# Kernel tuning notes

Measured on AMD Instinct MI355X. Metric: run time of the kernel, lower is better.

Reference implementation:

```python
import jax, jax.numpy as jnp
import numpy as np

B, N, C = 4, 262144, 10
K_PRE, K_POST = 4096, 500          # before_nms_max, after_nms_max
ROI_THR, NMS_THR = 0.1, 0.01       # roi_threshold, nms_threshold


def setup_inputs() -> dict:
    key = jax.random.key(0)
    k1, k2, k3, k4 = jax.random.split(key, 4)
    # raw logits; sigmoid(-2 + noise) straddles roi_threshold=0.1 realistically
    cls = jax.random.normal(k1, (B, N, C), jnp.float32) - 2.0
    centers = jax.random.uniform(k2, (B, N, 3), jnp.float32, minval=-50.0, maxval=50.0)
    sizes = jax.random.uniform(k3, (B, N, 3), jnp.float32, minval=0.5, maxval=5.0)
    heading = jax.random.uniform(k4, (B, N, 1), jnp.float32, minval=-np.pi, maxval=np.pi)
    boxes = jnp.concatenate([centers, sizes, heading], axis=-1)  # (B, N, 7)
    return {"batch_cls_preds": cls, "batch_box_preds": boxes}


def _pairwise_bev_iou(b):
    # b: (K, 7) = [x, y, z, dx, dy, dz, heading]; BEV IoU (heading ignored,
    # axis-aligned approximation of the rotated-IoU CUDA kernel).
    x, y, dx, dy = b[:, 0], b[:, 1], b[:, 3], b[:, 4]
    x1, x2 = x - dx * 0.5, x + dx * 0.5
    y1, y2 = y - dy * 0.5, y + dy * 0.5
    ix = jnp.clip(jnp.minimum(x2[:, None], x2[None, :]) - jnp.maximum(x1[:, None], x1[None, :]), 0.0)
    iy = jnp.clip(jnp.minimum(y2[:, None], y2[None, :]) - jnp.maximum(y1[:, None], y1[None, :]), 0.0)
    inter = ix * iy                              # (K, K)
    area = dx * dy                               # (K,)
    union = area[:, None] + area[None, :] - inter
    return inter / jnp.maximum(union, 1e-6)


def _nms_one(scores, labels, boxes):
    # scores: (N,), labels: (N,) int32, boxes: (N, 7)
    s = jnp.where(scores > ROI_THR, scores, -1.0)       # score-threshold filter
    topv, topi = jax.lax.top_k(s, K_PRE)                # keep top before_nms_max
    tb = boxes[topi]                                     # (K_PRE, 7)
    tl = labels[topi]
    iou = _pairwise_bev_iou(tb)                          # (K_PRE, K_PRE)
    keep0 = topv > ROI_THR

    def body(i, keep):
        # a kept higher-score box i suppresses later boxes with IoU > thr
        sup = (iou[i] > NMS_THR) & (jnp.arange(K_PRE) > i) & keep[i]
        return keep & ~sup

    keep = jax.lax.fori_loop(0, K_PRE, body, keep0)
    kept_scores = jnp.where(keep, topv, -1.0)
    fv, fi = jax.lax.top_k(kept_scores, K_POST)          # after_nms_max slots
    m = fv > 0.0
    final_scores = jnp.where(m, fv, 0.0)                 # (K_POST,)
    final_boxes = tb[fi] * m[:, None].astype(tb.dtype)   # (K_POST, 7)
    final_labels = jnp.where(m, tl[fi], -1)              # (K_POST,)
    return final_scores, final_boxes, final_labels


def reference(batch_cls_preds, batch_box_preds):
    probs = jax.nn.sigmoid(batch_cls_preds)              # (B, N, C)
    scores = jnp.max(probs, axis=-1)                     # per-anchor best class score
    labels = jnp.argmax(probs, axis=-1).astype(jnp.int32)
    final_scores, final_boxes, final_labels = jax.vmap(_nms_one)(scores, labels, batch_box_preds)
    return final_scores, final_boxes, final_labels
```

## Files before the change

kernel.cpp:

```cpp
#include <hip/hip_runtime.h>
#include <stdint.h>

constexpr int B = 4;
constexpr int N = 262144;
constexpr int C = 10;
constexpr int KPRE = 4096;
constexpr int KPOST = 500;
constexpr float ROI_THR = 0.1f;
constexpr float NMS_THR = 0.01f;
constexpr int CAP = 8192;
constexpr int MASKW = KPRE / 64;
constexpr int RJT = 2;
constexpr int MAXP = 32;

__device__ __forceinline__ uint32_t f2k(float f) {
  uint32_t u = __float_as_uint(f);
  return (u & 0x80000000u) ? ~u : (u | 0x80000000u);
}
__device__ __forceinline__ float k2f(uint32_t k) {
  uint32_t u = (k & 0x80000000u) ? (k ^ 0x80000000u) : ~k;
  return __uint_as_float(u);
}
__device__ __forceinline__ float sigm(float x) { return 1.0f / (1.0f + expf(-x)); }

__device__ __forceinline__ void async_lds16(const void* g, void* l) {
  __builtin_amdgcn_global_load_lds((const __attribute__((address_space(1))) void*)g,
                                   (__attribute__((address_space(3))) void*)l, 16, 0, 0);
}

__device__ __forceinline__ uint2 select256(const uint32_t* __restrict__ h, uint32_t R,
                                           uint32_t* s, uint32_t* o2) {
  int t = threadIdx.x;
  s[t] = h[t];
  __syncthreads();
  for (int off = 1; off < 256; off <<= 1) {
    uint32_t v = s[t] + ((t + off < 256) ? s[t + off] : 0u);
    __syncthreads();
    s[t] = v;
    __syncthreads();
  }
  uint32_t suf = s[t];
  uint32_t sufn = (t < 255) ? s[t + 1] : 0u;
  if (suf >= R && R > sufn) {
    o2[0] = (uint32_t)t;
    o2[1] = R - sufn;
  }
  __syncthreads();
  uint2 r;
  r.x = o2[0];
  r.y = o2[1];
  __syncthreads();
  return r;
}

__global__ void scoreK(const float* __restrict__ cls, uint32_t* __restrict__ keys,
                       uint32_t* __restrict__ hist0) {
  __shared__ float ls[2560];
  __shared__ uint32_t h[256];
  int b = blockIdx.y;
  int t = threadIdx.x;
  h[t] = 0;
  size_t base = ((size_t)b * N + (size_t)blockIdx.x * 256) * C;
  const float2* g2 = (const float2*)(cls + base);
  float2* l2 = (float2*)ls;
#pragma unroll
  for (int r = 0; r < 5; ++r) l2[r * 256 + t] = g2[r * 256 + t];
  __syncthreads();
  const float* mine = ls + t * 10;
  float m = mine[0];
#pragma unroll
  for (int c = 1; c < C; ++c) m = fmaxf(m, mine[c]);
  float p = sigm(m);
  float sc = (p > ROI_THR) ? p : -1.0f;
  uint32_t k = f2k(sc);
  keys[(size_t)b * N + blockIdx.x * 256 + t] = k;
  atomicAdd(&h[k >> 24], 1u);
  __syncthreads();
  if (h[t]) atomicAdd(&hist0[b * 256 + t], h[t]);
}

__global__ void histP1K(const uint32_t* __restrict__ keys, const uint32_t* __restrict__ hist0,
                        uint32_t* __restrict__ hist1) {
  __shared__ uint32_t s[256];
  __shared__ uint32_t o2[2];
  __shared__ uint32_t h[256];
  int b = blockIdx.y;
  int t = threadIdx.x;
  uint2 s0 = select256(hist0 + b * 256, (uint32_t)KPRE, s, o2);
  h[t] = 0;
  __syncthreads();
  uint32_t pref = s0.x;
  const uint4* kb4 = (const uint4*)(keys + (size_t)b * N);
#pragma unroll
  for (int r = 0; r < 2; ++r) {
    uint4 kv = kb4[blockIdx.x * 512 + r * 256 + t];
#pragma unroll
    for (int j = 0; j < 4; ++j) {
      uint32_t k = (&kv.x)[j];
      if ((k >> 24) == pref) atomicAdd(&h[(k >> 16) & 255u], 1u);
    }
  }
  __syncthreads();
  if (h[t]) atomicAdd(&hist1[b * 256 + t], h[t]);
}

__global__ void compactK(const uint32_t* __restrict__ keys, const uint32_t* __restrict__ hist0,
                         const uint32_t* __restrict__ hist1, unsigned long long* __restrict__ list,
                         uint32_t* __restrict__ cnt) {
  __shared__ uint32_t s[256];
  __shared__ uint32_t o2[2];
  __shared__ uint32_t scan[256];
  __shared__ uint32_t baseSh;
  int b = blockIdx.y;
  int t = threadIdx.x;
  uint2 s0 = select256(hist0 + b * 256, (uint32_t)KPRE, s, o2);
  uint2 s1 = select256(hist1 + b * 256, s0.y, s, o2);
  uint32_t T = ((s0.x << 8) | s1.x) << 16;
  const uint4* kb4 = (const uint4*)(keys + (size_t)b * N);
  uint4 kv[4];
#pragma unroll
  for (int r = 0; r < 4; ++r) kv[r] = kb4[blockIdx.x * 1024 + r * 256 + t];
  uint32_t c = 0;
#pragma unroll
  for (int r = 0; r < 4; ++r)
#pragma unroll
    for (int j = 0; j < 4; ++j) c += ((&kv[r].x)[j] >= T) ? 1u : 0u;
  scan[t] = c;
  __syncthreads();
  for (int off = 1; off < 256; off <<= 1) {
    uint32_t v = scan[t] + ((t >= off) ? scan[t - off] : 0u);
    __syncthreads();
    scan[t] = v;
    __syncthreads();
  }
  uint32_t excl = scan[t] - c;
  if (t == 255) baseSh = atomicAdd(&cnt[b], scan[255]);
  __syncthreads();
  uint32_t pos = baseSh + excl;
#pragma unroll
  for (int r = 0; r < 4; ++r)
#pragma unroll
    for (int j = 0; j < 4; ++j) {
      uint32_t k = (&kv[r].x)[j];
      if (k >= T) {
        uint32_t n = (blockIdx.x * 1024 + r * 256 + t) * 4 + j;
        if (pos < CAP)
          list[(size_t)b * CAP + pos] = ((unsigned long long)k << 32) | (uint32_t)(~n);
        pos++;
      }
    }
}

__global__ void rankK(const unsigned long long* __restrict__ list, const uint32_t* __restrict__ cnt,
                      uint32_t* __restrict__ rank) {
  __shared__ unsigned long long lp[256];
  int b = blockIdx.z;
  int cc = (int)min(cnt[b], (uint32_t)CAP);
  if (blockIdx.x * 256 >= cc) return;
  int j0 = blockIdx.y * (256 * RJT);
  if (j0 >= cc) return;
  int i = blockIdx.x * 256 + threadIdx.x;
  unsigned long long pi = (i < cc) ? list[(size_t)b * CAP + i] : ~0ull;
  uint32_t c = 0;
#pragma unroll
  for (int tb = 0; tb < RJT; ++tb) {
    int j = j0 + tb * 256 + threadIdx.x;
    __syncthreads();
    lp[threadIdx.x] = (j < cc) ? list[(size_t)b * CAP + j] : 0ull;
    __syncthreads();
#pragma unroll 8
    for (int jj = 0; jj < 256; ++jj) c += (lp[jj] > pi) ? 1u : 0u;
  }
  if (i < cc && c) atomicAdd(&rank[(size_t)b * CAP + i], c);
}

__global__ void scatterK(const unsigned long long* __restrict__ list,
                         const uint32_t* __restrict__ cnt, const uint32_t* __restrict__ rank,
                         const float* __restrict__ boxes, float* __restrict__ sel_score,
                         uint32_t* __restrict__ sel_idx, float* __restrict__ sel_box) {
  int b = blockIdx.y;
  int p = blockIdx.x * 256 + threadIdx.x;
  uint32_t cc = min(cnt[b], (uint32_t)CAP);
  if (p >= (int)cc) return;
  unsigned long long pk = list[(size_t)b * CAP + p];
  uint32_t r = rank[(size_t)b * CAP + p];
  if (r >= (uint32_t)KPRE) return;
  uint32_t key = (uint32_t)(pk >> 32);
  uint32_t idx = ~(uint32_t)pk;
  sel_score[b * KPRE + r] = k2f(key);
  sel_idx[b * KPRE + r] = idx;
  const float* src = boxes + ((size_t)b * N + idx) * 7;
  float* dst = sel_box + ((size_t)b * KPRE + r) * 8;
#pragma unroll
  for (int c = 0; c < 7; ++c) dst[c] = src[c];
  dst[7] = 0.f;
}

__global__ void maskK(const float* __restrict__ sel_box, unsigned long long* __restrict__ maskT,
                      unsigned long long* __restrict__ Tmat) {
  int b = blockIdx.z;
  int bi = blockIdx.x;
  int w = blockIdx.y;
  int t = threadIdx.x;
  int i = bi * 256 + t;
  int j0 = w * 64;
  if (j0 + 63 <= bi * 256) return;
  __shared__ float4 jv[64];
  __shared__ float ja[64];
  if (t < 64) {
    const float4* bj = (const float4*)(sel_box + ((size_t)b * KPRE + j0 + t) * 8);
    float4 lo = bj[0], hi = bj[1];
    float xj = lo.x, yj = lo.y, dxj = lo.w, dyj = hi.x;
    float hxj = __fmul_rn(dxj, 0.5f), hyj = __fmul_rn(dyj, 0.5f);
    float4 v;
    v.x = __fsub_rn(xj, hxj);
    v.y = __fadd_rn(xj, hxj);
    v.z = __fsub_rn(yj, hyj);
    v.w = __fadd_rn(yj, hyj);
    jv[t] = v;
    ja[t] = __fmul_rn(dxj, dyj);
  }
  __syncthreads();
  const float4* myb = (const float4*)(sel_box + ((size_t)b * KPRE + i) * 8);
  float4 lo = myb[0], hi = myb[1];
  float x = lo.x, y = lo.y, dx = lo.w, dy = hi.x;
  float hx = __fmul_rn(dx, 0.5f), hy = __fmul_rn(dy, 0.5f);
  float x1i = __fsub_rn(x, hx), x2i = __fadd_rn(x, hx);
  float y1i = __fsub_rn(y, hy), y2i = __fadd_rn(y, hy);
  float ai = __fmul_rn(dx, dy);
  unsigned long long wacc = 0ull;
#pragma unroll 16
  for (int jj = 0; jj < 64; ++jj) {
    int j = j0 + jj;
    float4 v = jv[jj];
    float aj = ja[jj];
    float xx1 = fmaxf(x1i, v.x);
    float xx2 = fminf(x2i, v.y);
    float yy1 = fmaxf(y1i, v.z);
    float yy2 = fminf(y2i, v.w);
    float ix = fmaxf(__fsub_rn(xx2, xx1), 0.0f);
    float iy = fmaxf(__fsub_rn(yy2, yy1), 0.0f);
    float inter = __fmul_rn(ix, iy);
    float den = fmaxf(__fsub_rn(__fadd_rn(ai, aj), inter), 1e-6f);
    float q0 = __fmul_rn(NMS_THR, den);
    float d = __fsub_rn(inter, q0);
    bool sup = d > 0.0f;
    if (__builtin_expect(__any(fabsf(d) <= q0 * 1e-5f), 0)) {
      sup = (inter / den) > NMS_THR;
    }
    sup = sup && (j > i);
    wacc |= ((unsigned long long)(sup ? 1u : 0u)) << jj;
  }
  maskT[((size_t)b * MASKW + w) * KPRE + i] = wacc;
  if ((w >> 2) == bi && (t >> 6) == (w & 3)) {
    int l = t & 63;
    unsigned long long m = wacc;
    unsigned long long T = 0ull;
#pragma unroll
    for (int j = 0; j < 64; ++j) {
      unsigned long long bj = __ballot(((m >> j) & 1ull) != 0ull);
      if (l == j) T = bj;
    }
    unsigned long long* trow = Tmat + ((size_t)b * 64 + w) * 128;
    trow[l] = T;
    trow[64 + l] = m;
  }
}

__global__ void nmsK(const unsigned long long* __restrict__ maskT,
                     const unsigned long long* __restrict__ Tmat,
                     const float* __restrict__ sel_score,
                     uint32_t* __restrict__ kept_pos, uint32_t* __restrict__ kept_cnt) {
  __shared__ unsigned long long td[64][128];
  __shared__ uint32_t keptbuf[KPOST];
  int b = blockIdx.x;
  int t = threadIdx.x;

  const char* tsrc = (const char*)(Tmat + (size_t)b * 64 * 128);
  for (int g = 0; g < 64; ++g)
    async_lds16(tsrc + (size_t)g * 1024 + (size_t)t * 16, &td[g][0]);

  unsigned long long cand = 0ull;
  for (int k = 0; k < 64; ++k) {
    float s = sel_score[b * KPRE + k * 64 + t];
    unsigned long long bal = __ballot(s > ROI_THR);
    if (t == k) cand = bal;
  }
  asm volatile("s_waitcnt vmcnt(0)" ::: "memory");

  const unsigned long long* mbt = maskT + (size_t)b * KPRE * MASKW + (size_t)t * KPRE;
  unsigned long long remv = 0ull;
  unsigned long long r[MAXP];
#pragma unroll
  for (int a = 0; a < MAXP; ++a) r[a] = 0ull;
  int kc = 0;

  for (int g = 0; g < 64; ++g) {
#pragma unroll
    for (int a = 0; a < MAXP; ++a) remv |= r[a];

    unsigned long long cw = cand & ~remv;
    unsigned long long aw =
        ((unsigned long long)(uint32_t)__builtin_amdgcn_readlane((uint32_t)(cw >> 32), g) << 32) |
        (uint32_t)__builtin_amdgcn_readlane((uint32_t)cw, g);
    if (aw) {
      unsigned long long T = td[g][t];
      unsigned long long m = td[g][64 + t];
      unsigned long long K = __ballot((m & aw) != 0ull);
      unsigned long long alive = aw;
      unsigned long long rem = aw & K;
      if (rem) {
        bool deadf = ((aw >> t) & 1ull) == 0ull;
        while (rem) {
          int s = __ffsll((long long)rem) - 1;
          rem &= rem - 1ull;
          if ((alive >> s) & 1ull) {
            deadf = deadf || (((T >> s) & 1ull) != 0ull);
            alive = __ballot(!deadf);
            rem &= alive;
          }
        }
      }
      int grp = __popcll(alive);
      if ((alive >> t) & 1ull) {
        int rk = __popcll(alive & ((1ull << t) - 1ull));
        if (kc + rk < KPOST) keptbuf[kc + rk] = (uint32_t)(g * 64 + t);
      }
      kc += grp;
      unsigned long long a2 = alive;
      bool again = true;
      while (again) {
#pragma unroll
        for (int a = 0; a < MAXP; ++a) {
          if (a2) {
            int s2 = __ffsll((long long)a2) - 1;
            a2 &= a2 - 1ull;
            r[a] = mbt[g * 64 + s2];
          } else {
            r[a] = 0ull;
          }
        }
        if (a2) {
#pragma unroll
          for (int a = 0; a < MAXP; ++a) {
            remv |= r[a];
            r[a] = 0ull;
          }
          again = true;
        } else {
          again = false;
        }
      }
      if (kc >= KPOST) break;
    } else {
#pragma unroll
      for (int a = 0; a < MAXP; ++a) r[a] = 0ull;
    }
  }
  asm volatile("s_waitcnt vmcnt(0)" ::: "memory");
  int kcc = min(kc, KPOST);
  for (int i = t; i < kcc; i += 64) kept_pos[b * KPOST + i] = keptbuf[i];
  if (t == 0) kept_cnt[b] = (uint32_t)kcc;
}

__global__ void outK(const float* __restrict__ cls,
                     const float* __restrict__ sel_score, const uint32_t* __restrict__ sel_idx,
                     const float* __restrict__ sel_box,
                     const uint32_t* __restrict__ kept_pos, const uint32_t* __restrict__ kept_cnt,
                     float* __restrict__ out) {
  int b = blockIdx.y;
  int s = blockIdx.x * blockDim.x + threadIdx.x;
  if (s >= KPOST) return;
  float* oS = out;
  float* oB = out + B * KPOST;
  float* oL = out + B * KPOST + B * KPOST * 7;
  uint32_t kcnt = kept_cnt[b];
  if (s < (int)kcnt) {
    uint32_t pos = kept_pos[b * KPOST + s];
    oS[b * KPOST + s] = sel_score[b * KPRE + pos];
    const float* box = sel_box + ((size_t)b * KPRE + pos) * 8;
    float* dst = oB + ((size_t)b * KPOST + s) * 7;
#pragma unroll
    for (int c = 0; c < 7; ++c) dst[c] = box[c];
    uint32_t idx = sel_idx[b * KPRE + pos];
    const float* p = cls + ((size_t)b * N + idx) * C;
    float bestv = sigm(p[0]);
    int bestc = 0;
#pragma unroll
    for (int c = 1; c < C; ++c) {
      float v = sigm(p[c]);
      if (v > bestv) { bestv = v; bestc = c; }
    }
    oL[b * KPOST + s] = (float)bestc;
  } else {
    oS[b * KPOST + s] = 0.0f;
    float* dst = oB + ((size_t)b * KPOST + s) * 7;
#pragma unroll
    for (int c = 0; c < 7; ++c) dst[c] = 0.0f;
    oL[b * KPOST + s] = -1.0f;
  }
}

__global__ void sentinelK(float* out, int n) {
  int i = blockIdx.x * blockDim.x + threadIdx.x;
  if (i < n) out[i] = 1337.0f;
}

extern "C" void kernel_launch(void* const* d_in, const int* in_sizes, int n_in,
                              void* d_out, int out_size, void* d_ws, size_t ws_size,
                              hipStream_t stream) {
  const float* cls = (const float*)d_in[0];
  const float* boxes = (const float*)d_in[1];
  float* out = (float*)d_out;

  char* ws = (char*)d_ws;
  size_t off = 0;
  auto alloc = [&](size_t bytes) -> void* {
    void* p = ws + off;
    off = (off + bytes + 255) & ~(size_t)255;
    return p;
  };
  size_t mask_bytes = (size_t)B * KPRE * MASKW * 8;
  unsigned long long* mask = (unsigned long long*)alloc(mask_bytes);
  unsigned long long* list = (unsigned long long*)alloc((size_t)B * CAP * 8);
  uint32_t* keys = (uint32_t*)alloc((size_t)B * N * 4);
  float* sel_box = (float*)alloc((size_t)B * KPRE * 8 * 4);
  float* sel_score = (float*)alloc((size_t)B * KPRE * 4);
  uint32_t* sel_idx = (uint32_t*)alloc((size_t)B * KPRE * 4);
  uint32_t* kept_pos = (uint32_t*)alloc((size_t)B * KPOST * 4);
  uint32_t* kept_cnt = (uint32_t*)alloc(B * 4);
  unsigned long long* Tmat = (unsigned long long*)alloc((size_t)B * 64 * 128 * 8);

  uint32_t* hist0 = (uint32_t*)mask;
  uint32_t* hist1 = hist0 + B * 256;
  uint32_t* cnt = hist1 + B * 256;
  uint32_t* rank = (uint32_t*)((char*)mask + 16384);

  if (off > ws_size) {
    sentinelK<<<dim3((out_size + 255) / 256), 256, 0, stream>>>(out, out_size);
    return;
  }

  hipMemsetAsync(mask, 0, mask_bytes, stream);
  scoreK<<<dim3(N / 256, B), 256, 0, stream>>>(cls, keys, hist0);
  histP1K<<<dim3(N / 2048, B), 256, 0, stream>>>(keys, hist0, hist1);
  compactK<<<dim3(N / 4096, B), 256, 0, stream>>>(keys, hist0, hist1, list, cnt);
  rankK<<<dim3(CAP / 256, CAP / (256 * RJT), B), 256, 0, stream>>>(list, cnt, rank);
  scatterK<<<dim3(CAP / 256, B), 256, 0, stream>>>(list, cnt, rank, boxes, sel_score, sel_idx,
                                                   sel_box);
  maskK<<<dim3(16, 64, B), 256, 0, stream>>>(sel_box, mask, Tmat);
  nmsK<<<B, 64, 0, stream>>>(mask, Tmat, sel_score, kept_pos, kept_cnt);
  outK<<<dim3((KPOST + 255) / 256, B), 256, 0, stream>>>(cls, sel_score, sel_idx, sel_box,
                                                         kept_pos, kept_cnt, out);
}
```

Before: 146.6 us.

## Shrink maskK blocks to one wave, skip lower-triangle tiles, hoist ambiguity check

The IoU mask kernel now uses 64-thread blocks covering one 64x64 tile, so every tile below the diagonal is skipped outright instead of only whole 256-row groups. The j>i comparison is compiled only for diagonal tiles through a template. The per-element wave vote on near-threshold values is replaced by one accumulated flag and a single vote after the loop, with an exact-division recompute of the tile when it fires. This cuts redundant IoU work and per-iteration cross-lane votes, at the cost of four times as many small blocks and an occasional full recompute pass.

```diff
diff --git a/kernel.cpp b/kernel.cpp
--- a/kernel.cpp
+++ b/kernel.cpp
@@ -196,18 +196,43 @@
   dst[7] = 0.f;
 }
 
-__global__ void maskK(const float* __restrict__ sel_box, unsigned long long* __restrict__ maskT,
-                      unsigned long long* __restrict__ Tmat) {
+template <bool CHK>
+__device__ __forceinline__ void mask_row64(int tt, const float4* __restrict__ jv,
+                                           const float* __restrict__ ja, float x1i, float x2i,
+                                           float y1i, float y2i, float ai, uint32_t& lo0,
+                                           uint32_t& hi0, uint32_t& band) {
+#pragma unroll 16
+  for (int jj = 0; jj < 64; ++jj) {
+    float4 v = jv[jj];
+    float aj = ja[jj];
+    float xx1 = fmaxf(x1i, v.x), xx2 = fminf(x2i, v.y);
+    float yy1 = fmaxf(y1i, v.z), yy2 = fminf(y2i, v.w);
+    float ix = fmaxf(__fsub_rn(xx2, xx1), 0.0f), iy = fmaxf(__fsub_rn(yy2, yy1), 0.0f);
+    float inter = __fmul_rn(ix, iy);
+    float den = fmaxf(__fsub_rn(__fadd_rn(ai, aj), inter), 1e-6f);
+    float q0 = __fmul_rn(NMS_THR, den);
+    float d = __fsub_rn(inter, q0);
+    band |= (fabsf(d) <= __fmul_rn(q0, 1e-5f)) ? 1u : 0u;
+    bool sup = d > 0.0f;
+    if (CHK) sup = sup && (jj > tt);
+    uint32_t bit = sup ? 1u : 0u;
+    if (jj < 32) lo0 |= bit << jj; else hi0 |= bit << (jj - 32);
+  }
+}
+
+__global__ __launch_bounds__(64) void maskK(const float* __restrict__ sel_box,
+                                            unsigned long long* __restrict__ maskT,
+                                            unsigned long long* __restrict__ Tmat) {
   int b = blockIdx.z;
   int bi = blockIdx.x;
   int w = blockIdx.y;
-  int t = threadIdx.x;
-  int i = bi * 256 + t;
+  if (w < bi) return;
+  int t = threadIdx.x;
+  int i = bi * 64 + t;
   int j0 = w * 64;
-  if (j0 + 63 <= bi * 256) return;
   __shared__ float4 jv[64];
   __shared__ float ja[64];
-  if (t < 64) {
+  {
     const float4* bj = (const float4*)(sel_box + ((size_t)b * KPRE + j0 + t) * 8);
     float4 lo = bj[0], hi = bj[1];
     float xj = lo.x, yj = lo.y, dxj = lo.w, dyj = hi.x;
@@ -228,42 +253,39 @@
   float x1i = __fsub_rn(x, hx), x2i = __fadd_rn(x, hx);
   float y1i = __fsub_rn(y, hy), y2i = __fadd_rn(y, hy);
   float ai = __fmul_rn(dx, dy);
-  unsigned long long wacc = 0ull;
-#pragma unroll 16
-  for (int jj = 0; jj < 64; ++jj) {
-    int j = j0 + jj;
-    float4 v = jv[jj];
-    float aj = ja[jj];
-    float xx1 = fmaxf(x1i, v.x);
-    float xx2 = fminf(x2i, v.y);
-    float yy1 = fmaxf(y1i, v.z);
-    float yy2 = fminf(y2i, v.w);
-    float ix = fmaxf(__fsub_rn(xx2, xx1), 0.0f);
-    float iy = fmaxf(__fsub_rn(yy2, yy1), 0.0f);
-    float inter = __fmul_rn(ix, iy);
-    float den = fmaxf(__fsub_rn(__fadd_rn(ai, aj), inter), 1e-6f);
-    float q0 = __fmul_rn(NMS_THR, den);
-    float d = __fsub_rn(inter, q0);
-    bool sup = d > 0.0f;
-    if (__builtin_expect(__any(fabsf(d) <= q0 * 1e-5f), 0)) {
-      sup = (inter / den) > NMS_THR;
-    }
-    sup = sup && (j > i);
-    wacc |= ((unsigned long long)(sup ? 1u : 0u)) << jj;
-  }
+  uint32_t lo0 = 0, hi0 = 0, band = 0;
+  if (w == bi)
+    mask_row64<true>(t, jv, ja, x1i, x2i, y1i, y2i, ai, lo0, hi0, band);
+  else
+    mask_row64<false>(t, jv, ja, x1i, x2i, y1i, y2i, ai, lo0, hi0, band);
+  if (__builtin_expect(__any(band != 0), 0)) {
+    lo0 = hi0 = 0;
+    for (int jj = 0; jj < 64; ++jj) {
+      float4 v = jv[jj];
+      float aj = ja[jj];
+      float xx1 = fmaxf(x1i, v.x), xx2 = fminf(x2i, v.y);
+      float yy1 = fmaxf(y1i, v.z), yy2 = fminf(y2i, v.w);
+      float ix = fmaxf(__fsub_rn(xx2, xx1), 0.0f), iy = fmaxf(__fsub_rn(yy2, yy1), 0.0f);
+      float inter = __fmul_rn(ix, iy);
+      float den = fmaxf(__fsub_rn(__fadd_rn(ai, aj), inter), 1e-6f);
+      bool sup = (inter / den) > NMS_THR && (j0 + jj > i);
+      uint32_t bit = sup ? 1u : 0u;
+      if (jj < 32) lo0 |= bit << jj; else hi0 |= bit << (jj - 32);
+    }
+  }
+  unsigned long long wacc = ((unsigned long long)hi0 << 32) | lo0;
   maskT[((size_t)b * MASKW + w) * KPRE + i] = wacc;
-  if ((w >> 2) == bi && (t >> 6) == (w & 3)) {
-    int l = t & 63;
+  if (w == bi) {
     unsigned long long m = wacc;
     unsigned long long T = 0ull;
 #pragma unroll
     for (int j = 0; j < 64; ++j) {
       unsigned long long bj = __ballot(((m >> j) & 1ull) != 0ull);
-      if (l == j) T = bj;
+      if (t == j) T = bj;
     }
     unsigned long long* trow = Tmat + ((size_t)b * 64 + w) * 128;
-    trow[l] = T;
-    trow[64 + l] = m;
+    trow[t] = T;
+    trow[64 + t] = m;
   }
 }
 
@@ -448,7 +470,7 @@
   rankK<<<dim3(CAP / 256, CAP / (256 * RJT), B), 256, 0, stream>>>(list, cnt, rank);
   scatterK<<<dim3(CAP / 256, B), 256, 0, stream>>>(list, cnt, rank, boxes, sel_score, sel_idx,
                                                    sel_box);
-  maskK<<<dim3(16, 64, B), 256, 0, stream>>>(sel_box, mask, Tmat);
+  maskK<<<dim3(64, 64, B), 64, 0, stream>>>(sel_box, mask, Tmat);
   nmsK<<<B, 64, 0, stream>>>(mask, Tmat, sel_score, kept_pos, kept_cnt);
   outK<<<dim3((KPOST + 255) / 256, B), 256, 0, stream>>>(cls, sel_score, sel_idx, sel_box,
                                                          kept_pos, kept_cnt, out);
```

Measured after the change: 140.4 us. 4.2% less time.
